# Optimization experiments

Hardware: AMD Instinct MI355X
Metric: run time of the kernel (lower is better)

## Reference

```python
import jax, jax.numpy as jnp
import numpy as np

B, IN, HID, OUT, MH = 32, 784, 256, 128, 32
RATE = 1e-3


def setup_inputs() -> dict:
    key = jax.random.key(0)
    ks = jax.random.split(key, 6)
    def w(k, shape, fan_in):
        return (jax.random.normal(k, shape, jnp.float32) / np.sqrt(fan_in)).astype(jnp.float32)
    return {
        "x": jax.random.normal(ks[0], (B, IN), jnp.float32),
        "W1": w(ks[1], (HID, IN), IN),
        "b1": jnp.zeros((HID,), jnp.float32),
        "W2": w(ks[2], (OUT, HID), HID),
        "b2": jnp.zeros((OUT,), jnp.float32),
        "mW1": w(ks[3], (MH, 3), 3),
        "mb1": jnp.zeros((MH,), jnp.float32),
        "mW2": w(ks[4], (1, MH), MH),
        "mb2": jnp.zeros((1,), jnp.float32),
        "batch_num": 1,
    }


def _meta(feats, mW1, mb1, mW2, mb2):
    # feats: [B, O, I, 3] -> scalar shift per (b, j, i)
    h = jax.nn.relu(jnp.einsum("boif,hf->boih", feats, mW1) + mb1)
    return (jnp.einsum("boih,kh->boik", h, mW2) + mb2)[..., 0]  # [B, O, I]


def _layer_step(out, W, b, mW1, mb1, mW2, mb2, scale):
    vi = out                                   # [B, I]
    vj = jax.nn.relu(out @ W.T + b)            # [B, O]
    # features per (batch, out-neuron, in-neuron): (input act, weight, output act)
    feats = jnp.stack(
        jnp.broadcast_arrays(vi[:, None, :], W[None, :, :], vj[:, :, None]),
        axis=-1,
    )  # [B, O, I, 3]
    shift = _meta(feats, mW1, mb1, mW2, mb2) * scale   # [B, O, I]
    new_out = vj + jnp.einsum("bi,boi->bo", vi, shift)  # weighted reduce over inputs
    W_new = W + jnp.mean(shift, axis=0)                 # hebbian-style weight update
    return new_out, W_new


def reference(x, W1, b1, W2, b2, mW1, mb1, mW2, mb2, batch_num):
    scale = RATE / batch_num
    out1, W1_new = _layer_step(x, W1, b1, mW1, mb1, mW2, mb2, scale)
    out2, W2_new = _layer_step(out1, W2, b2, mW1, mb1, mW2, mb2, scale)
    return out2, W1_new, W2_new
```

## Files before the change

kernel.cpp:

```cpp
#include <hip/hip_runtime.h>

#define B_   32
#define IN_  784
#define HID_ 256
#define OUT_ 128
#define MH_  32
#define RATE_ 1e-3f

#define OFF_OUT1  0
#define OFF_XT    8192
#define OFF_O1T   33280
#define OFF_VJ1T  41472
#define OFF_VJ2T  49664

__global__ void kA(const float* __restrict__ x, const float* __restrict__ W1,
                   const float* __restrict__ b1, float* __restrict__ ws) {
    float* out1 = ws + OFF_OUT1;
    float* xT   = ws + OFF_XT;
    float* vjT1 = ws + OFF_VJ1T;
    int t = threadIdx.x, blk = blockIdx.x;

    if (blk < 98) {
        int e = blk * 256 + t;
        int i = e >> 5, b = e & 31;
        xT[e] = x[b * IN_ + i];
    }

    int lane = t & 63;
    int p = blk * 4 + (t >> 6);
    int b = p >> 8, o = p & 255;
    const float4* xr4 = (const float4*)(x  + b * IN_);
    const float4* wr4 = (const float4*)(W1 + o * IN_);
    float acc = 0.f;
    #pragma unroll
    for (int k = 0; k < 3; ++k) {
        float4 xa = xr4[lane + 64 * k];
        float4 wa = wr4[lane + 64 * k];
        acc = fmaf(xa.x, wa.x, acc); acc = fmaf(xa.y, wa.y, acc);
        acc = fmaf(xa.z, wa.z, acc); acc = fmaf(xa.w, wa.w, acc);
    }
    if (lane < 4) {
        float4 xa = xr4[192 + lane];
        float4 wa = wr4[192 + lane];
        acc = fmaf(xa.x, wa.x, acc); acc = fmaf(xa.y, wa.y, acc);
        acc = fmaf(xa.z, wa.z, acc); acc = fmaf(xa.w, wa.w, acc);
    }
    #pragma unroll
    for (int m = 1; m < 64; m <<= 1) acc += __shfl_xor(acc, m, 64);
    if (lane == 0) {
        float v = fmaxf(acc + b1[o], 0.f);
        out1[p] = v;
        vjT1[o * 32 + b] = v;
    }
}

template<int IN_DIM, int OUT_DIM, int NCH, int IBLK>
__global__ __launch_bounds__(128)
void layer_main(const float* __restrict__ viT,
                const float* __restrict__ W,
                const float* __restrict__ vjT,
                const float* __restrict__ mW1, const float* __restrict__ mb1,
                const float* __restrict__ mW2, const float* __restrict__ mb2,
                const int*   __restrict__ batch_num,
                float* __restrict__ Wnew,
                float* __restrict__ outAcc)
{
    __shared__ float osh[32 * 129];
    __shared__ float psh[128];

    int t = threadIdx.x;
    int o  = blockIdx.x / NCH;
    int il = t;
    bool act = (IBLK == 128) || (il < IBLK);
    int i = (blockIdx.x % NCH) * IBLK + (act ? il : 0);

    float wv = act ? W[o * IN_DIM + i] : 0.f;

    float vi[32];
    {
        const float4* vp = (const float4*)(viT + i * 32);
        #pragma unroll
        for (int k = 0; k < 8; ++k) {
            float4 v4 = act ? vp[k] : make_float4(0.f, 0.f, 0.f, 0.f);
            vi[4*k+0] = v4.x; vi[4*k+1] = v4.y; vi[4*k+2] = v4.z; vi[4*k+3] = v4.w;
        }
    }

    float vjv[32];
    {
        const float* vp = vjT + o * 32;
        #pragma unroll
        for (int k = 0; k < 32; ++k) vjv[k] = vp[k];
    }

    float s[32];
    #pragma unroll
    for (int k = 0; k < 32; ++k) s[k] = 0.f;

    #pragma unroll 8
    for (int h = 0; h < MH_; ++h) {
        float a  = mW1[3*h + 0];
        float bw = mW1[3*h + 1];
        float c  = mW1[3*h + 2];
        float w2 = mW2[h];
        float base = fmaf(bw, wv, mb1[h]);
        #pragma unroll
        for (int bb = 0; bb < 32; ++bb) {
            float pre = fmaf(c, vjv[bb], base);
            float tt  = fmaf(a, vi[bb], pre);
            tt = fmaxf(tt, 0.f);
            s[bb] = fmaf(w2, tt, s[bb]);
        }
    }

    float scale = RATE_ / (float)batch_num[0];
    float mb2v  = mb2[0];
    float wsum = 0.f;
    #pragma unroll
    for (int bb = 0; bb < 32; ++bb) {
        float sh = (s[bb] + mb2v) * scale;
        wsum += sh;
        osh[bb * 129 + t] = vi[bb] * sh;
    }
    if (act) Wnew[o * IN_DIM + i] = wv + wsum * 0.03125f;

    __syncthreads();
    {
        int b = t & 31, seg = t >> 5;
        const float* row = osh + b * 129 + seg * 32;
        float p = 0.f;
        #pragma unroll
        for (int k = 0; k < 32; ++k) p += row[k];
        psh[t] = p;
    }
    __syncthreads();
    if (t < 32) {
        float v = psh[t] + psh[32 + t] + psh[64 + t] + psh[96 + t];
        atomicAdd(&outAcc[t * OUT_DIM + o], v);
    }
}

__global__ void kC(const float* __restrict__ out1, const float* __restrict__ W2,
                   const float* __restrict__ b2, float* __restrict__ vj2T,
                   float* __restrict__ o1T, float* __restrict__ out2) {
    int t = threadIdx.x, blk = blockIdx.x;

    if (blk < 32) {
        int e = blk * 256 + t;
        int i = e >> 5, b = e & 31;
        o1T[e] = out1[b * HID_ + i];
    }

    int lane = t & 63;
    int p = blk * 4 + (t >> 6);
    int b = p >> 7, o = p & 127;
    const float4* xr4 = (const float4*)(out1 + b * HID_);
    const float4* wr4 = (const float4*)(W2   + b * 0 + o * HID_);
    float4 xa = xr4[lane];
    float4 wa = wr4[lane];
    float acc = fmaf(xa.x, wa.x, fmaf(xa.y, wa.y, fmaf(xa.z, wa.z, xa.w * wa.w)));
    #pragma unroll
    for (int m = 1; m < 64; m <<= 1) acc += __shfl_xor(acc, m, 64);
    if (lane == 0) {
        float v = fmaxf(acc + b2[o], 0.f);
        out2[p]          = v;
        vj2T[o * 32 + b] = v;
    }
}

extern "C" void kernel_launch(void* const* d_in, const int* in_sizes, int n_in,
                              void* d_out, int out_size, void* d_ws, size_t ws_size,
                              hipStream_t stream) {
    const float* x   = (const float*)d_in[0];
    const float* W1  = (const float*)d_in[1];
    const float* b1  = (const float*)d_in[2];
    const float* W2  = (const float*)d_in[3];
    const float* b2  = (const float*)d_in[4];
    const float* mW1 = (const float*)d_in[5];
    const float* mb1 = (const float*)d_in[6];
    const float* mW2 = (const float*)d_in[7];
    const float* mb2 = (const float*)d_in[8];
    const int* batch_num = (const int*)d_in[9];

    float* out2  = (float*)d_out;
    float* W1n   = out2 + B_ * OUT_;
    float* W2n   = W1n + HID_ * IN_;
    float* ws    = (float*)d_ws;

    kA<<<2048, 256, 0, stream>>>(x, W1, b1, ws);
    layer_main<IN_, HID_, 7, 112><<<HID_ * 7, 128, 0, stream>>>(
        ws + OFF_XT, W1, ws + OFF_VJ1T, mW1, mb1, mW2, mb2, batch_num,
        W1n, ws + OFF_OUT1);
    kC<<<1024, 256, 0, stream>>>(ws + OFF_OUT1, W2, b2,
                                 ws + OFF_VJ2T, ws + OFF_O1T, out2);
    layer_main<HID_, OUT_, 2, 128><<<OUT_ * 2, 128, 0, stream>>>(
        ws + OFF_O1T, W2, ws + OFF_VJ2T, mW1, mb1, mW2, mb2, batch_num,
        W2n, out2);
}
```

Before: 118.0 us.

## Remap layer kernel so lanes index batch and threads own few inputs

The meta-network layer kernel changes its thread mapping. Each lane now handles one batch element and each thread covers a small run of input neurons, where before each thread held all 32 batch values of a single input in registers. The meta-weights are staged in shared memory, and the vj-dependent term is folded once per hidden unit. The batch-mean weight update is now reduced with wave shuffles instead of a padded shared-memory transpose. This is meant to cut register pressure, raise occupancy and give the second layer more blocks, at the cost of shuffle reductions and gathered vi loads.

```diff
diff --git a/kernel.cpp b/kernel.cpp
--- a/kernel.cpp
+++ b/kernel.cpp
@@ -54,8 +54,8 @@
     }
 }
 
-template<int IN_DIM, int OUT_DIM, int NCH, int IBLK>
-__global__ __launch_bounds__(128)
+template<int IN_DIM, int OUT_DIM, int NCH, int CPT>
+__global__ __launch_bounds__(256)
 void layer_main(const float* __restrict__ viT,
                 const float* __restrict__ W,
                 const float* __restrict__ vjT,
@@ -65,77 +65,80 @@
                 float* __restrict__ Wnew,
                 float* __restrict__ outAcc)
 {
-    __shared__ float osh[32 * 129];
-    __shared__ float psh[128];
+    __shared__ float4 m4s[MH_];
+    __shared__ float  w2s[MH_];
+    __shared__ float  osh[4][32];
 
     int t = threadIdx.x;
+    int b = t & 31, g = t >> 5;
     int o  = blockIdx.x / NCH;
-    int il = t;
-    bool act = (IBLK == 128) || (il < IBLK);
-    int i = (blockIdx.x % NCH) * IBLK + (act ? il : 0);
-
-    float wv = act ? W[o * IN_DIM + i] : 0.f;
-
-    float vi[32];
-    {
-        const float4* vp = (const float4*)(viT + i * 32);
-        #pragma unroll
-        for (int k = 0; k < 8; ++k) {
-            float4 v4 = act ? vp[k] : make_float4(0.f, 0.f, 0.f, 0.f);
-            vi[4*k+0] = v4.x; vi[4*k+1] = v4.y; vi[4*k+2] = v4.z; vi[4*k+3] = v4.w;
+    int i0 = (blockIdx.x % NCH) * (8 * CPT) + g * CPT;
+
+    if (t < MH_) {
+        m4s[t] = make_float4(mW1[t*3+0], mW1[t*3+1], mW1[t*3+2], mb1[t]);
+        w2s[t] = mW2[t];
+    }
+    __syncthreads();
+
+    float vjv = vjT[o * 32 + b];
+
+    float vi[CPT], wv[CPT], s[CPT];
+    #pragma unroll
+    for (int k = 0; k < CPT; ++k) {
+        vi[k] = viT[(i0 + k) * 32 + b];
+        wv[k] = W[o * IN_DIM + i0 + k];
+        s[k]  = 0.f;
+    }
+
+    #pragma unroll
+    for (int hc = 0; hc < MH_ / 8; ++hc) {
+        float a[8], bw[8], w2[8], cvm[8];
+        #pragma unroll
+        for (int j = 0; j < 8; ++j) {
+            float4 m = m4s[hc * 8 + j];
+            a[j]   = m.x;
+            bw[j]  = m.y;
+            cvm[j] = fmaf(m.z, vjv, m.w);
+            w2[j]  = w2s[hc * 8 + j];
         }
-    }
-
-    float vjv[32];
-    {
-        const float* vp = vjT + o * 32;
-        #pragma unroll
-        for (int k = 0; k < 32; ++k) vjv[k] = vp[k];
-    }
-
-    float s[32];
-    #pragma unroll
-    for (int k = 0; k < 32; ++k) s[k] = 0.f;
-
-    #pragma unroll 8
-    for (int h = 0; h < MH_; ++h) {
-        float a  = mW1[3*h + 0];
-        float bw = mW1[3*h + 1];
-        float c  = mW1[3*h + 2];
-        float w2 = mW2[h];
-        float base = fmaf(bw, wv, mb1[h]);
-        #pragma unroll
-        for (int bb = 0; bb < 32; ++bb) {
-            float pre = fmaf(c, vjv[bb], base);
-            float tt  = fmaf(a, vi[bb], pre);
-            tt = fmaxf(tt, 0.f);
-            s[bb] = fmaf(w2, tt, s[bb]);
+        #pragma unroll
+        for (int k = 0; k < CPT; ++k) {
+            float vik = vi[k], wvk = wv[k];
+            #pragma unroll
+            for (int j = 0; j < 8; ++j) {
+                float tt = fmaf(a[j], vik, fmaf(bw[j], wvk, cvm[j]));
+                tt = fmaxf(tt, 0.f);
+                s[k] = fmaf(w2[j], tt, s[k]);
+            }
         }
     }
 
     float scale = RATE_ / (float)batch_num[0];
     float mb2v  = mb2[0];
-    float wsum = 0.f;
-    #pragma unroll
-    for (int bb = 0; bb < 32; ++bb) {
-        float sh = (s[bb] + mb2v) * scale;
-        wsum += sh;
-        osh[bb * 129 + t] = vi[bb] * sh;
-    }
-    if (act) Wnew[o * IN_DIM + i] = wv + wsum * 0.03125f;
-
-    __syncthreads();
-    {
-        int b = t & 31, seg = t >> 5;
-        const float* row = osh + b * 129 + seg * 32;
-        float p = 0.f;
-        #pragma unroll
-        for (int k = 0; k < 32; ++k) p += row[k];
-        psh[t] = p;
-    }
+    float outacc = 0.f;
+    float r[CPT];
+    #pragma unroll
+    for (int k = 0; k < CPT; ++k) {
+        float sh = (s[k] + mb2v) * scale;
+        outacc = fmaf(vi[k], sh, outacc);
+        r[k] = sh;
+    }
+    #pragma unroll
+    for (int mm = 1; mm < 32; mm <<= 1) {
+        #pragma unroll
+        for (int k = 0; k < CPT; ++k) r[k] += __shfl_xor(r[k], mm);
+    }
+    if (b == 0) {
+        #pragma unroll
+        for (int k = 0; k < CPT; ++k)
+            Wnew[o * IN_DIM + i0 + k] = wv[k] + r[k] * 0.03125f;
+    }
+
+    outacc += __shfl_xor(outacc, 32);
+    if ((t & 32) == 0) osh[t >> 6][b] = outacc;
     __syncthreads();
     if (t < 32) {
-        float v = psh[t] + psh[32 + t] + psh[64 + t] + psh[96 + t];
+        float v = osh[0][t] + osh[1][t] + osh[2][t] + osh[3][t];
         atomicAdd(&outAcc[t * OUT_DIM + o], v);
     }
 }
@@ -155,7 +158,7 @@
     int p = blk * 4 + (t >> 6);
     int b = p >> 7, o = p & 127;
     const float4* xr4 = (const float4*)(out1 + b * HID_);
-    const float4* wr4 = (const float4*)(W2   + b * 0 + o * HID_);
+    const float4* wr4 = (const float4*)(W2   + o * HID_);
     float4 xa = xr4[lane];
     float4 wa = wr4[lane];
     float acc = fmaf(xa.x, wa.x, fmaf(xa.y, wa.y, fmaf(xa.z, wa.z, xa.w * wa.w)));
@@ -188,12 +191,12 @@
     float* ws    = (float*)d_ws;
 
     kA<<<2048, 256, 0, stream>>>(x, W1, b1, ws);
-    layer_main<IN_, HID_, 7, 112><<<HID_ * 7, 128, 0, stream>>>(
+    layer_main<IN_, HID_, 7, 14><<<HID_ * 7, 256, 0, stream>>>(
         ws + OFF_XT, W1, ws + OFF_VJ1T, mW1, mb1, mW2, mb2, batch_num,
         W1n, ws + OFF_OUT1);
     kC<<<1024, 256, 0, stream>>>(ws + OFF_OUT1, W2, b2,
                                  ws + OFF_VJ2T, ws + OFF_O1T, out2);
-    layer_main<HID_, OUT_, 2, 128><<<OUT_ * 2, 128, 0, stream>>>(
+    layer_main<HID_, OUT_, 8, 4><<<OUT_ * 8, 256, 0, stream>>>(
         ws + OFF_O1T, W2, ws + OFF_VJ2T, mW1, mb1, mW2, mb2, batch_num,
         W2n, out2);
 }
```

Result: faster. 110.8 us (-6.1%).
